# Kernel tuning notes

Measured on AMD Instinct MI355X. Metric: run time of the kernel, lower is better.

## Reference

```python
import jax, jax.numpy as jnp
import numpy as np
from jax import lax

ROUTINGS = 3
SCALING = 2
NUM_CAPSULE = 8
NUM_ATOMS = 16
EPS = 1e-9


def squash(v):
    # SegCaps squash: v * |v|^2 / ((1+|v|^2) * |v|), norm over last axis
    sq = jnp.sum(v * v, axis=-1, keepdims=True)
    return v * sq / ((1.0 + sq) * jnp.sqrt(sq + EPS))


def setup_inputs() -> dict:
    key = jax.random.key(0)
    k1, k2 = jax.random.split(key)
    B, H, Wd, Cin, Ain = 4, 56, 56, 8, 32
    x = jax.random.normal(k1, (B, H, Wd, Cin, Ain), dtype=jnp.float32)
    # TF conv2d_transpose filter layout: [k, k, out_ch, in_ch]
    W = jax.random.normal(k2, (4, 4, NUM_CAPSULE * NUM_ATOMS, Ain), dtype=jnp.float32) * 0.05
    b = 0.1 * jnp.ones((1, 1, NUM_CAPSULE, NUM_ATOMS), dtype=jnp.float32)
    return {"x": x, "W": W, "b": b}


def reference(x, W, b):
    B, H, Wd, Cin, Ain = x.shape
    Cout, Aout = NUM_CAPSULE, NUM_ATOMS
    # [B,H,W,Cin,A] -> [Cin,B,H,W,A] -> [Cin*B,H,W,A]  (faithful to original ordering)
    xt = jnp.transpose(x, (3, 0, 1, 2, 4)).reshape(Cin * B, H, Wd, Ain)
    # TF conv2d_transpose, SAME padding, stride=scaling: out spatial = in * scaling
    out = lax.conv_transpose(
        xt, W, strides=(SCALING, SCALING), padding="SAME",
        dimension_numbers=("NHWC", "HWIO", "NHWC"), transpose_kernel=True)
    Hp, Wp = out.shape[1], out.shape[2]
    # votes: [B, Cin, Hp, Wp, Cout, Aout]  (faithful to original reshape)
    votes = out.reshape(B, Cin, Hp, Wp, Cout, Aout)
    biases = jnp.broadcast_to(b, (Hp, Wp, Cout, Aout))
    logits = jnp.zeros((B, Cin, Hp, Wp, Cout), dtype=x.dtype)
    act = None
    for i in range(ROUTINGS):
        route = jax.nn.softmax(logits, axis=-1)                      # [B,Cin,Hp,Wp,Cout]
        pre = jnp.einsum("bihwc,bihwca->bhwca", route, votes) + biases
        act = squash(pre)                                            # [B,Hp,Wp,Cout,Aout]
        if i < ROUTINGS - 1:
            logits = logits + jnp.einsum("bihwca,bhwca->bihwc", votes, act)
    return act
```

## Files before the change

kernel.cpp:

```cpp
#include <hip/hip_runtime.h>
#include <math.h>

#define CEPS 1e-9f

typedef _Float16 half8 __attribute__((ext_vector_type(8)));
typedef _Float16 h2 __attribute__((ext_vector_type(2)));
typedef __fp16 fp16x2 __attribute__((ext_vector_type(2)));
typedef float floatx16 __attribute__((ext_vector_type(16)));


template<int CTRL>
__device__ __forceinline__ float dpp_add(float v) {
    return v + __int_as_float(__builtin_amdgcn_update_dpp(
        0, __float_as_int(v), CTRL, 0xF, 0xF, false));
}
__device__ __forceinline__ h2 pkrtz(float a, float b) {
    return __builtin_bit_cast(h2, __builtin_amdgcn_cvt_pkrtz(a, b));
}
__device__ __forceinline__ float fdot2(h2 a, h2 b, float c) {
    return __builtin_amdgcn_fdot2(__builtin_bit_cast(fp16x2, a),
                                  __builtin_bit_cast(fp16x2, b), c, false);
}

__global__ __launch_bounds__(256) void prep_w(const float* __restrict__ Wt,
                                              _Float16* __restrict__ wb) {
    int idx = blockIdx.x * 256 + threadIdx.x;
    int parity = idx >> 11;
    int s = (idx >> 8) & 7;
    int t = (idx >> 6) & 3;
    int l = idx & 63;
    int rh = parity >> 1, rw = parity & 1;
    int n = t * 32 + (l & 31);
    int h = l >> 5;
    int ci0 = ((s & 1) << 4) + (h << 3);
    int kh = ((s >> 2) << 1) + 1 - rh;
    int kw = (((s >> 1) & 1) << 1) + 1 - rw;
    const float* src = Wt + (((kh * 4 + kw) * 128 + n) << 5) + ci0;
    float4 w0 = *(const float4*)src;
    float4 w1 = *(const float4*)(src + 4);
    half8 hv;
    hv[0] = (_Float16)w0.x; hv[1] = (_Float16)w0.y;
    hv[2] = (_Float16)w0.z; hv[3] = (_Float16)w0.w;
    hv[4] = (_Float16)w1.x; hv[5] = (_Float16)w1.y;
    hv[6] = (_Float16)w1.z; hv[7] = (_Float16)w1.w;
    *(half8*)(wb + ((long)idx << 3)) = hv;
}

__global__ __launch_bounds__(256, 5) void caps_mfma(
    const float* __restrict__ x,
    const _Float16* __restrict__ wb,
    const float* __restrict__ bias,
    float* __restrict__ out)
{
    __shared__ __align__(16) unsigned char smem[32768];
    _Float16* xt = (_Float16*)smem;
    _Float16* scxh = (_Float16*)smem;

    const int tid = threadIdx.x;
    const int tile = blockIdx.x;
    const int tu = tile / 14, tv = tile - tu * 14;
    const int u0 = tu * 4, v0 = tv * 4;
    const int rh = blockIdx.y >> 1;
    const int rw = blockIdx.y & 1;
    const int bp = blockIdx.z;
    const _Float16* wsrc = wb + ((long)blockIdx.y << 14);

    #pragma unroll
    for (int it = 0; it < 4; ++it) {
        int idx = tid + (it << 8);
        if (idx < 800) {
            int cell = idx >> 5;
            int r = idx & 31;
            int i = r >> 2;
            int ci0 = (r & 3) << 3;
            int ri = cell / 5, rj = cell - ri * 5;
            int gi = u0 + rh - 1 + ri;
            int gj = v0 + rw - 1 + rj;
            float tmp[8] = {0.f, 0.f, 0.f, 0.f, 0.f, 0.f, 0.f, 0.f};
            if ((unsigned)gi < 56u && (unsigned)gj < 56u) {
                const float* src = x + (((i & 3) * 56 + gi) * 56 + gj) * 256
                                     + ((bp * 2 + (i >> 2)) << 5) + ci0;
                float4 a0 = *(const float4*)src;
                float4 a1 = *(const float4*)(src + 4);
                tmp[0] = a0.x; tmp[1] = a0.y; tmp[2] = a0.z; tmp[3] = a0.w;
                tmp[4] = a1.x; tmp[5] = a1.y; tmp[6] = a1.z; tmp[7] = a1.w;
            }
            half8 hv;
            #pragma unroll
            for (int j = 0; j < 8; ++j) hv[j] = (_Float16)tmp[j];
            *(half8*)(xt + (cell * 8 + i) * 40 + ci0) = hv;
        }
    }
    __syncthreads();

    const int l = tid & 63;
    const int w = tid >> 6;
    const int col = l & 31, h = l >> 5;
    const int invA = (l & 31) * 40 + (h << 3);

    h2 pf[4][8];
    #pragma unroll
    for (int half = 0; half < 2; ++half) {
        floatx16 acc0, acc1;
        #pragma unroll
        for (int j = 0; j < 16; ++j) { acc0[j] = 0.f; acc1[j] = 0.f; }
        const int tb = half << 1;
        #pragma unroll
        for (int s = 0; s < 8; ++s) {
            const int tkh = s >> 2;
            const int tkw = (s >> 1) & 1;
            const int row = w + 1 - tkh;
            int aoff = (row * 5 + 1 - tkw) * 320 + ((s & 1) << 4) + invA;
            asm("" : "+v"(aoff));
            half8 af = *(const half8*)(xt + aoff);
            half8 bf0 = *(const half8*)(wsrc + (((s * 4 + tb) * 64 + l) << 3));
            half8 bf1 = *(const half8*)(wsrc + (((s * 4 + tb + 1) * 64 + l) << 3));
            acc0 = __builtin_amdgcn_mfma_f32_32x32x16_f16(af, bf0, acc0, 0, 0, 0);
            acc1 = __builtin_amdgcn_mfma_f32_32x32x16_f16(af, bf1, acc1, 0, 0, 0);
        }
        #pragma unroll
        for (int m = 0; m < 8; ++m) {
            pf[tb][m]     = pkrtz(acc0[2 * m], acc0[2 * m + 1]);
            pf[tb + 1][m] = pkrtz(acc1[2 * m], acc1[2 * m + 1]);
        }
        __builtin_amdgcn_sched_barrier(0);
    }

    __syncthreads();

    _Float16* wbW = scxh + (w << 12);
    {
        _Float16* wp = wbW + (h << 9) + col;
        #pragma unroll
        for (int t = 0; t < 4; ++t)
            #pragma unroll
            for (int m = 0; m < 8; ++m) {
                h2 pp = pf[t][m];
                const int pixl = m >> 1;
                const int il0 = (2 * m) & 3;
                const int il1 = (2 * m + 1) & 3;
                wp[pixl * 1024 + il0 * 128 + t * 32] = pp[0];
                wp[pixl * 1024 + il1 * 128 + t * 32] = pp[1];
            }
    }

    const int e = l & 1;
    const int c = (l >> 1) & 7;
    const int pl = l >> 4;

    h2 va[8][4];
    {
        const _Float16* rp = wbW + (pl << 10) + (c << 4) + (e << 3);
        #pragma unroll
        for (int i = 0; i < 8; ++i) {
            half8 vv = *(const half8*)(rp + (i << 7));
            va[i][0][0] = vv[0]; va[i][0][1] = vv[1];
            va[i][1][0] = vv[2]; va[i][1][1] = vv[3];
            va[i][2][0] = vv[4]; va[i][2][1] = vv[5];
            va[i][3][0] = vv[6]; va[i][3][1] = vv[7];
        }
    }

    h2 bq[4];
    {
        const float* bpt = bias + (c << 4) + (e << 3);
        float4 b0 = *(const float4*)bpt;
        float4 b1 = *(const float4*)(bpt + 4);
        bq[0] = pkrtz(b0.x, b0.y); bq[1] = pkrtz(b0.z, b0.w);
        bq[2] = pkrtz(b1.x, b1.y); bq[3] = pkrtz(b1.z, b1.w);
    }
    const h2 c0125 = pkrtz(0.125f, 0.125f);

    h2 pre[4];
    float lgv[8];

    #pragma unroll
    for (int d = 0; d < 4; ++d) {
        h2 s01 = va[0][d] + va[1][d];
        h2 s23 = va[2][d] + va[3][d];
        h2 s45 = va[4][d] + va[5][d];
        h2 s67 = va[6][d] + va[7][d];
        h2 s = (s01 + s23) + (s45 + s67);
        pre[d] = s * c0125 + bq[d];
    }
    {
        float n = fdot2(pre[0], pre[0], 0.f);
        n = fdot2(pre[1], pre[1], n);
        n = fdot2(pre[2], pre[2], n);
        n = fdot2(pre[3], pre[3], n);
        float nq = dpp_add<0xB1>(n);
        float sc = nq * __builtin_amdgcn_rcpf(1.f + nq)
                      * __builtin_amdgcn_rsqf(nq + CEPS);
        h2 sc2 = pkrtz(sc, sc);
        #pragma unroll
        for (int d = 0; d < 4; ++d) pre[d] *= sc2;
    }
    #pragma unroll
    for (int i = 0; i < 8; ++i) {
        float p = fdot2(va[i][0], pre[0], 0.f);
        p = fdot2(va[i][1], pre[1], p);
        p = fdot2(va[i][2], pre[2], p);
        p = fdot2(va[i][3], pre[3], p);
        lgv[i] = dpp_add<0xB1>(p);
    }

    #pragma unroll
    for (int r = 1; r < 3; ++r) {
        h2 rt2[8];
        #pragma unroll
        for (int i = 0; i < 8; ++i) {
            float ee = __expf(lgv[i]);
            float ss = dpp_add<0x4E>(ee);
            ss = dpp_add<0x141>(ss);
            ss = dpp_add<0x128>(ss);
            float route = ee * __builtin_amdgcn_rcpf(ss);
            rt2[i] = pkrtz(route, route);
        }
        #pragma unroll
        for (int d = 0; d < 4; ++d) {
            h2 p0 = rt2[0] * va[0][d], p1 = rt2[1] * va[1][d];
            h2 p2 = rt2[2] * va[2][d], p3 = rt2[3] * va[3][d];
            h2 p4 = rt2[4] * va[4][d], p5 = rt2[5] * va[5][d];
            h2 p6 = rt2[6] * va[6][d], p7 = rt2[7] * va[7][d];
            h2 s = ((p0 + p1) + (p2 + p3)) + ((p4 + p5) + (p6 + p7));
            pre[d] = s + bq[d];
        }
        {
            float n = fdot2(pre[0], pre[0], 0.f);
            n = fdot2(pre[1], pre[1], n);
            n = fdot2(pre[2], pre[2], n);
            n = fdot2(pre[3], pre[3], n);
            float nq = dpp_add<0xB1>(n);
            float sc = nq * __builtin_amdgcn_rcpf(1.f + nq)
                          * __builtin_amdgcn_rsqf(nq + CEPS);
            h2 sc2 = pkrtz(sc, sc);
            #pragma unroll
            for (int d = 0; d < 4; ++d) pre[d] *= sc2;
        }
        if (r < 2) {
            #pragma unroll
            for (int i = 0; i < 8; ++i) {
                float p = fdot2(va[i][0], pre[0], 0.f);
                p = fdot2(va[i][1], pre[1], p);
                p = fdot2(va[i][2], pre[2], p);
                p = fdot2(va[i][3], pre[3], p);
                lgv[i] += dpp_add<0xB1>(p);
            }
        }
    }

    {
        const int p = ((u0 + w) << 1) + rh;
        const int q = ((v0 + pl) << 1) + rw;
        float* op = out + (((bp * 112 + p) * 112 + q) << 7) + (c << 4) + (e << 3);
        float4 o0 = make_float4((float)pre[0][0], (float)pre[0][1],
                                (float)pre[1][0], (float)pre[1][1]);
        float4 o1 = make_float4((float)pre[2][0], (float)pre[2][1],
                                (float)pre[3][0], (float)pre[3][1]);
        *(float4*)op = o0;
        *(float4*)(op + 4) = o1;
    }
}

extern "C" void kernel_launch(void* const* d_in, const int* in_sizes, int n_in,
                              void* d_out, int out_size, void* d_ws, size_t ws_size,
                              hipStream_t stream) {
    const float* x  = (const float*)d_in[0];
    const float* Wt = (const float*)d_in[1];
    const float* b  = (const float*)d_in[2];
    float* out = (float*)d_out;
    _Float16* wb = (_Float16*)d_ws;

    prep_w<<<32, 256, 0, stream>>>(Wt, wb);
    dim3 grid(196, 4, 4);
    caps_mfma<<<grid, 256, 0, stream>>>(x, wb, b, out);
}
```

Baseline: 103.3 us.

## Stream first-half MFMA votes to LDS instead of holding them in registers

```diff
diff --git a/kernel.cpp b/kernel.cpp
--- a/kernel.cpp
+++ b/kernel.cpp
@@ -54,7 +54,7 @@
 {
     __shared__ __align__(16) unsigned char smem[32768];
     _Float16* xt = (_Float16*)smem;
-    _Float16* scxh = (_Float16*)smem;
+    _Float16* smem16 = (_Float16*)smem;
 
     const int tid = threadIdx.x;
     const int tile = blockIdx.x;
@@ -98,13 +98,25 @@
     const int col = l & 31, h = l >> 5;
     const int invA = (l & 31) * 40 + (h << 3);
 
-    h2 pf[4][8];
-    #pragma unroll
-    for (int half = 0; half < 2; ++half) {
+    const int e = l & 1;
+    const int c = (l >> 1) & 7;
+    const int pl = l >> 4;
+
+    h2 bq[4];
+    {
+        const float* bpt = bias + (c << 4) + (e << 3);
+        float4 b0 = *(const float4*)bpt;
+        float4 b1 = *(const float4*)(bpt + 4);
+        bq[0] = pkrtz(b0.x, b0.y); bq[1] = pkrtz(b0.z, b0.w);
+        bq[2] = pkrtz(b1.x, b1.y); bq[3] = pkrtz(b1.z, b1.w);
+    }
+
+    #pragma unroll
+    for (int hf = 0; hf < 2; ++hf) {
         floatx16 acc0, acc1;
         #pragma unroll
         for (int j = 0; j < 16; ++j) { acc0[j] = 0.f; acc1[j] = 0.f; }
-        const int tb = half << 1;
+        const int tb = hf << 1;
         #pragma unroll
         for (int s = 0; s < 8; ++s) {
             const int tkh = s >> 2;
@@ -118,57 +130,38 @@
             acc0 = __builtin_amdgcn_mfma_f32_32x32x16_f16(af, bf0, acc0, 0, 0, 0);
             acc1 = __builtin_amdgcn_mfma_f32_32x32x16_f16(af, bf1, acc1, 0, 0, 0);
         }
+        if (hf == 1) __syncthreads();
+        _Float16* dst = smem16 + (hf ? 0 : 8192) + w * 2048;
         #pragma unroll
         for (int m = 0; m < 8; ++m) {
-            pf[tb][m]     = pkrtz(acc0[2 * m], acc0[2 * m + 1]);
-            pf[tb + 1][m] = pkrtz(acc1[2 * m], acc1[2 * m + 1]);
+            h2 q0 = pkrtz(acc0[2 * m], acc0[2 * m + 1]);
+            h2 q1 = pkrtz(acc1[2 * m], acc1[2 * m + 1]);
+            const int mpl = m >> 1;
+            const int il0 = (2 * m) & 3;
+            const int il1 = (2 * m + 1) & 3;
+            const int r0 = (mpl * 8 + 4 * h + il0) * 64 + col;
+            const int r1 = (mpl * 8 + 4 * h + il1) * 64 + col;
+            dst[r0]      = q0[0];
+            dst[r1]      = q0[1];
+            dst[r0 + 32] = q1[0];
+            dst[r1 + 32] = q1[1];
         }
         __builtin_amdgcn_sched_barrier(0);
     }
 
-    __syncthreads();
-
-    _Float16* wbW = scxh + (w << 12);
-    {
-        _Float16* wp = wbW + (h << 9) + col;
-        #pragma unroll
-        for (int t = 0; t < 4; ++t)
-            #pragma unroll
-            for (int m = 0; m < 8; ++m) {
-                h2 pp = pf[t][m];
-                const int pixl = m >> 1;
-                const int il0 = (2 * m) & 3;
-                const int il1 = (2 * m + 1) & 3;
-                wp[pixl * 1024 + il0 * 128 + t * 32] = pp[0];
-                wp[pixl * 1024 + il1 * 128 + t * 32] = pp[1];
-            }
-    }
-
-    const int e = l & 1;
-    const int c = (l >> 1) & 7;
-    const int pl = l >> 4;
+    const _Float16* rp = smem16 + (c < 4 ? 8192 : 0) + w * 2048
+                       + (pl << 9) + ((c & 3) << 4) + (e << 3);
 
     h2 va[8][4];
-    {
-        const _Float16* rp = wbW + (pl << 10) + (c << 4) + (e << 3);
-        #pragma unroll
-        for (int i = 0; i < 8; ++i) {
-            half8 vv = *(const half8*)(rp + (i << 7));
-            va[i][0][0] = vv[0]; va[i][0][1] = vv[1];
-            va[i][1][0] = vv[2]; va[i][1][1] = vv[3];
-            va[i][2][0] = vv[4]; va[i][2][1] = vv[5];
-            va[i][3][0] = vv[6]; va[i][3][1] = vv[7];
-        }
-    }
-
-    h2 bq[4];
-    {
-        const float* bpt = bias + (c << 4) + (e << 3);
-        float4 b0 = *(const float4*)bpt;
-        float4 b1 = *(const float4*)(bpt + 4);
-        bq[0] = pkrtz(b0.x, b0.y); bq[1] = pkrtz(b0.z, b0.w);
-        bq[2] = pkrtz(b1.x, b1.y); bq[3] = pkrtz(b1.z, b1.w);
-    }
+    #pragma unroll
+    for (int i = 0; i < 8; ++i) {
+        half8 vv = *(const half8*)(rp + (i << 6));
+        va[i][0][0] = vv[0]; va[i][0][1] = vv[1];
+        va[i][1][0] = vv[2]; va[i][1][1] = vv[3];
+        va[i][2][0] = vv[4]; va[i][2][1] = vv[5];
+        va[i][3][0] = vv[6]; va[i][3][1] = vv[7];
+    }
+
     const h2 c0125 = pkrtz(0.125f, 0.125f);
 
     h2 pre[4];
```

New measurement: 103.2 us. Within noise of the previous version (-0.0%).

## Fuse weight fp16 conversion into main kernel via LDS staging, drop prep kernel

Applied to the files above, without the earlier changes.

```diff
diff --git a/kernel.cpp b/kernel.cpp
--- a/kernel.cpp
+++ b/kernel.cpp
@@ -22,39 +22,16 @@
                                   __builtin_bit_cast(fp16x2, b), c, false);
 }
 
-__global__ __launch_bounds__(256) void prep_w(const float* __restrict__ Wt,
-                                              _Float16* __restrict__ wb) {
-    int idx = blockIdx.x * 256 + threadIdx.x;
-    int parity = idx >> 11;
-    int s = (idx >> 8) & 7;
-    int t = (idx >> 6) & 3;
-    int l = idx & 63;
-    int rh = parity >> 1, rw = parity & 1;
-    int n = t * 32 + (l & 31);
-    int h = l >> 5;
-    int ci0 = ((s & 1) << 4) + (h << 3);
-    int kh = ((s >> 2) << 1) + 1 - rh;
-    int kw = (((s >> 1) & 1) << 1) + 1 - rw;
-    const float* src = Wt + (((kh * 4 + kw) * 128 + n) << 5) + ci0;
-    float4 w0 = *(const float4*)src;
-    float4 w1 = *(const float4*)(src + 4);
-    half8 hv;
-    hv[0] = (_Float16)w0.x; hv[1] = (_Float16)w0.y;
-    hv[2] = (_Float16)w0.z; hv[3] = (_Float16)w0.w;
-    hv[4] = (_Float16)w1.x; hv[5] = (_Float16)w1.y;
-    hv[6] = (_Float16)w1.z; hv[7] = (_Float16)w1.w;
-    *(half8*)(wb + ((long)idx << 3)) = hv;
-}
-
 __global__ __launch_bounds__(256, 5) void caps_mfma(
     const float* __restrict__ x,
-    const _Float16* __restrict__ wb,
+    const float* __restrict__ Wt,
     const float* __restrict__ bias,
     float* __restrict__ out)
 {
     __shared__ __align__(16) unsigned char smem[32768];
-    _Float16* xt = (_Float16*)smem;
-    _Float16* scxh = (_Float16*)smem;
+    _Float16* xt   = (_Float16*)smem;
+    _Float16* wt16 = (_Float16*)(smem + 16384);
+    _Float16* scx  = (_Float16*)smem;
 
     const int tid = threadIdx.x;
     const int tile = blockIdx.x;
@@ -63,7 +40,6 @@
     const int rh = blockIdx.y >> 1;
     const int rw = blockIdx.y & 1;
     const int bp = blockIdx.z;
-    const _Float16* wsrc = wb + ((long)blockIdx.y << 14);
 
     #pragma unroll
     for (int it = 0; it < 4; ++it) {
@@ -91,6 +67,28 @@
             *(half8*)(xt + (cell * 8 + i) * 40 + ci0) = hv;
         }
     }
+
+    #pragma unroll
+    for (int k = 0; k < 4; ++k) {
+        int en = tid + (k << 8);
+        int s  = en >> 7;
+        int t  = (en >> 6) & 1;
+        int ll = en & 63;
+        int n  = t * 32 + (ll & 31);
+        int hh = ll >> 5;
+        int ci0 = ((s & 1) << 4) + (hh << 3);
+        int kh = ((s >> 2) << 1) + 1 - rh;
+        int kw = (((s >> 1) & 1) << 1) + 1 - rw;
+        const float* src = Wt + (((kh * 4 + kw) * 128 + n) << 5) + ci0;
+        float4 w0 = *(const float4*)src;
+        float4 w1 = *(const float4*)(src + 4);
+        half8 hv;
+        hv[0] = (_Float16)w0.x; hv[1] = (_Float16)w0.y;
+        hv[2] = (_Float16)w0.z; hv[3] = (_Float16)w0.w;
+        hv[4] = (_Float16)w1.x; hv[5] = (_Float16)w1.y;
+        hv[6] = (_Float16)w1.z; hv[7] = (_Float16)w1.w;
+        *(half8*)(wt16 + (en << 3)) = hv;
+    }
     __syncthreads();
 
     const int l = tid & 63;
@@ -98,13 +96,25 @@
     const int col = l & 31, h = l >> 5;
     const int invA = (l & 31) * 40 + (h << 3);
 
+    const int e = l & 1;
+    const int c = (l >> 1) & 7;
+    const int pl = l >> 4;
+    h2 bq[4];
+    {
+        const float* bpt = bias + (c << 4) + (e << 3);
+        float4 b0 = *(const float4*)bpt;
+        float4 b1 = *(const float4*)(bpt + 4);
+        bq[0] = pkrtz(b0.x, b0.y); bq[1] = pkrtz(b0.z, b0.w);
+        bq[2] = pkrtz(b1.x, b1.y); bq[3] = pkrtz(b1.z, b1.w);
+    }
+
     h2 pf[4][8];
     #pragma unroll
-    for (int half = 0; half < 2; ++half) {
+    for (int hf = 0; hf < 2; ++hf) {
         floatx16 acc0, acc1;
         #pragma unroll
         for (int j = 0; j < 16; ++j) { acc0[j] = 0.f; acc1[j] = 0.f; }
-        const int tb = half << 1;
+        const int tb = hf << 1;
         #pragma unroll
         for (int s = 0; s < 8; ++s) {
             const int tkh = s >> 2;
@@ -113,8 +123,14 @@
             int aoff = (row * 5 + 1 - tkw) * 320 + ((s & 1) << 4) + invA;
             asm("" : "+v"(aoff));
             half8 af = *(const half8*)(xt + aoff);
-            half8 bf0 = *(const half8*)(wsrc + (((s * 4 + tb) * 64 + l) << 3));
-            half8 bf1 = *(const half8*)(wsrc + (((s * 4 + tb + 1) * 64 + l) << 3));
+
+            int boff0 = ((((s << 1) + 0) * 64 + l) << 4);
+            int boff1 = ((((s << 1) + 1) * 64 + l) << 4);
+            asm volatile("" : "+v"(boff0));
+            asm volatile("" : "+v"(boff1));
+            half8 bf0 = *(const half8*)((const unsigned char*)wt16 + boff0);
+            half8 bf1 = *(const half8*)((const unsigned char*)wt16 + boff1);
+
             acc0 = __builtin_amdgcn_mfma_f32_32x32x16_f16(af, bf0, acc0, 0, 0, 0);
             acc1 = __builtin_amdgcn_mfma_f32_32x32x16_f16(af, bf1, acc1, 0, 0, 0);
         }
@@ -124,11 +140,36 @@
             pf[tb + 1][m] = pkrtz(acc1[2 * m], acc1[2 * m + 1]);
         }
         __builtin_amdgcn_sched_barrier(0);
+        if (hf == 0) {
+            __syncthreads();
+            #pragma unroll
+            for (int k = 0; k < 4; ++k) {
+                int en = tid + (k << 8);
+                int s  = en >> 7;
+                int t  = (en >> 6) & 1;
+                int ll = en & 63;
+                int n  = (t + 2) * 32 + (ll & 31);
+                int hh = ll >> 5;
+                int ci0 = ((s & 1) << 4) + (hh << 3);
+                int kh = ((s >> 2) << 1) + 1 - rh;
+                int kw = (((s >> 1) & 1) << 1) + 1 - rw;
+                const float* src = Wt + (((kh * 4 + kw) * 128 + n) << 5) + ci0;
+                float4 w0 = *(const float4*)src;
+                float4 w1 = *(const float4*)(src + 4);
+                half8 hv;
+                hv[0] = (_Float16)w0.x; hv[1] = (_Float16)w0.y;
+                hv[2] = (_Float16)w0.z; hv[3] = (_Float16)w0.w;
+                hv[4] = (_Float16)w1.x; hv[5] = (_Float16)w1.y;
+                hv[6] = (_Float16)w1.z; hv[7] = (_Float16)w1.w;
+                *(half8*)(wt16 + (en << 3)) = hv;
+            }
+            __syncthreads();
+        }
     }
 
     __syncthreads();
 
-    _Float16* wbW = scxh + (w << 12);
+    _Float16* wbW = scx + (w << 12);
     {
         _Float16* wp = wbW + (h << 9) + col;
         #pragma unroll
@@ -136,17 +177,13 @@
             #pragma unroll
             for (int m = 0; m < 8; ++m) {
                 h2 pp = pf[t][m];
-                const int pixl = m >> 1;
+                const int mpl = m >> 1;
                 const int il0 = (2 * m) & 3;
                 const int il1 = (2 * m + 1) & 3;
-                wp[pixl * 1024 + il0 * 128 + t * 32] = pp[0];
-                wp[pixl * 1024 + il1 * 128 + t * 32] = pp[1];
+                wp[mpl * 1024 + il0 * 128 + t * 32] = pp[0];
+                wp[mpl * 1024 + il1 * 128 + t * 32] = pp[1];
             }
     }
-
-    const int e = l & 1;
-    const int c = (l >> 1) & 7;
-    const int pl = l >> 4;
 
     h2 va[8][4];
     {
@@ -161,16 +198,7 @@
         }
     }
 
-    h2 bq[4];
-    {
-        const float* bpt = bias + (c << 4) + (e << 3);
-        float4 b0 = *(const float4*)bpt;
-        float4 b1 = *(const float4*)(bpt + 4);
-        bq[0] = pkrtz(b0.x, b0.y); bq[1] = pkrtz(b0.z, b0.w);
-        bq[2] = pkrtz(b1.x, b1.y); bq[3] = pkrtz(b1.z, b1.w);
-    }
     const h2 c0125 = pkrtz(0.125f, 0.125f);
-
     h2 pre[4];
     float lgv[8];
 
@@ -269,9 +297,8 @@
     const float* Wt = (const float*)d_in[1];
     const float* b  = (const float*)d_in[2];
     float* out = (float*)d_out;
-    _Float16* wb = (_Float16*)d_ws;
-
-    prep_w<<<32, 256, 0, stream>>>(Wt, wb);
+    (void)d_ws; (void)ws_size;
+
     dim3 grid(196, 4, 4);
-    caps_mfma<<<grid, 256, 0, stream>>>(x, wb, b, out);
-}
+    caps_mfma<<<grid, 256, 0, stream>>>(x, Wt, b, out);
+}
```

Result: slower. 109.1 us (+5.6%).
